# Optimization experiments

Measured on AMD Instinct MI355X. Metric: run time of the kernel, lower is better.

## Reference

```python
import jax, jax.numpy as jnp
import numpy as np

# NOTE: the original source omits the definitions of QSVT, quantum_lcu_block,
# QuantumSumBlock and KANLayer. We reconstruct the standard math these blocks
# implement in quantum-KAN papers/repos:
#   QSVT(x)            -> vector of Chebyshev polynomials T_1..T_D of the
#                         (squashed) input, the polynomial basis QSVT realizes.
#   quantum_lcu_block  -> linear combination of unitaries: weighted sum of the
#                         QSVT vector normalized by the LCU l1 weight norm.
#   QuantumSumBlock    -> learnable interference sum: mean_k sin(alpha_k * v).
#   KANLayer           -> Chebyshev-KAN layer: spline term (Chebyshev basis
#                         contracted with coeffs) + SiLU base branch + bias.
# Everything is fully vectorized over (B, F) instead of the original per-scalar
# Python loops.

B, F, DEG, C, KBASIS = 16384, 512, 8, 10, 8


def _cheb(x, K):
    """Chebyshev features T_1..T_K of x in (-1, 1): shape x.shape + (K,)."""
    t = jnp.arccos(jnp.clip(x, -1.0, 1.0))
    k = jnp.arange(1, K + 1, dtype=x.dtype)
    return jnp.cos(t[..., None] * k)


def setup_inputs() -> dict:
    key = jax.random.key(0)
    ks = jax.random.split(key, 6)
    return {
        "X": jax.random.normal(ks[0], (B, F), dtype=jnp.float32),
        # nn.Parameter(torch.rand(num_features, degree))
        "lcu_weights": jax.random.uniform(ks[1], (F, DEG), dtype=jnp.float32),
        # one QuantumSumBlock(degree) per feature -> (F, DEG) phases
        "sum_alpha": jax.random.normal(ks[2], (F, DEG), dtype=jnp.float32),
        # KANLayer params
        "kan_coeff": jax.random.normal(ks[3], (C, F, KBASIS), dtype=jnp.float32) * 0.1,
        "kan_base": jax.random.normal(ks[4], (C, F), dtype=jnp.float32) * 0.1,
        "kan_bias": jnp.zeros((C,), dtype=jnp.float32),
    }


def reference(X, lcu_weights, sum_alpha, kan_coeff, kan_base, kan_bias):
    # squash inputs into the open interval (-1, 1) for the Chebyshev/QSVT basis
    x = 0.99 * jnp.tanh(X)                                   # (B, F)
    # QSVT polynomial feature vector per scalar, batched: (B, F, DEG)
    qsvt = _cheb(x, lcu_weights.shape[1])
    # LCU block: weighted combination normalized by l1 norm of weights -> (B, F)
    lcu = jnp.einsum('bfd,fd->bf', qsvt, lcu_weights) / (
        jnp.sum(jnp.abs(lcu_weights), axis=-1) + 1e-8)
    # Quantum sum block: learnable sinusoidal interference sum -> (B, F)
    summed = jnp.mean(jnp.sin(lcu[..., None] * sum_alpha), axis=-1)
    # Chebyshev-KAN layer
    s = 0.99 * jnp.tanh(summed)
    phi = _cheb(s, kan_coeff.shape[2])                       # (B, F, KBASIS)
    logits = (jnp.einsum('bfk,cfk->bc', phi, kan_coeff)
              + jax.nn.silu(summed) @ kan_base.T
              + kan_bias)                                    # (B, C)
    return logits
```

## Files before the change

### kernel.cpp

```cpp
#include <hip/hip_runtime.h>

#define BATCH 16384
#define NF    512
#define DEG   8
#define NC    10
#define KB    8

#define SPLITF 8
#define FC     (NF / SPLITF)
#define RB     64
#define PITCH  65
#define NT     256
#define NWAVES 4
#define FPW    (FC / NWAVES)

__device__ __forceinline__ float fast_tanh(float x) {
    float e = __expf(2.0f * x);
    return 1.0f - 2.0f * __builtin_amdgcn_rcpf(e + 1.0f);
}
__device__ __forceinline__ float fast_sigmoid(float x) {
    return __builtin_amdgcn_rcpf(1.0f + __expf(-x));
}

__global__ __launch_bounds__(256) void init_out(const float* __restrict__ bias,
                                                float* __restrict__ out) {
    int i = blockIdx.x * 256 + threadIdx.x;
    if (i < BATCH * NC) out[i] = bias[i % NC];
}

__global__ __launch_bounds__(NT) void qkan_kernel(
    const float* __restrict__ X,
    const float* __restrict__ lcu_w,
    const float* __restrict__ alpha,
    const float* __restrict__ coeff,
    const float* __restrict__ base,
    float* __restrict__ out)
{
    __shared__ float s_mem[RB * PITCH];

    const int t      = threadIdx.x;
    const int rowblk = blockIdx.x >> 3;
    const int fsplit = blockIdx.x & (SPLITF - 1);
    const int row0   = rowblk * RB;
    const int fbase  = fsplit * FC;
    const int wave   = __builtin_amdgcn_readfirstlane(t >> 6);
    const int lane   = t & 63;

    {
        const int f2   = t & 31;
        const int rsub = t >> 5;
        const int fA   = fbase + f2 * 2;

        float w[2][DEG], a[2][DEG], rden[2];
#pragma unroll
        for (int i = 0; i < 2; ++i) {
            const float4 w0 = *(const float4*)(lcu_w + (fA + i) * DEG);
            const float4 w1 = *(const float4*)(lcu_w + (fA + i) * DEG + 4);
            const float4 a0 = *(const float4*)(alpha + (fA + i) * DEG);
            const float4 a1 = *(const float4*)(alpha + (fA + i) * DEG + 4);
            w[i][0]=w0.x; w[i][1]=w0.y; w[i][2]=w0.z; w[i][3]=w0.w;
            w[i][4]=w1.x; w[i][5]=w1.y; w[i][6]=w1.z; w[i][7]=w1.w;
            a[i][0]=a0.x; a[i][1]=a0.y; a[i][2]=a0.z; a[i][3]=a0.w;
            a[i][4]=a1.x; a[i][5]=a1.y; a[i][6]=a1.z; a[i][7]=a1.w;
            float den = 1e-8f;
#pragma unroll
            for (int d = 0; d < DEG; ++d) den += fabsf(w[i][d]);
            rden[i] = __builtin_amdgcn_rcpf(den);
        }

#pragma unroll
        for (int it = 0; it < RB / 8; ++it) {
            const int r = rsub + it * 8;
            const float2 xv = *(const float2*)(X + (row0 + r) * NF + fA);
            float xs[2] = {xv.x, xv.y};
#pragma unroll
            for (int i = 0; i < 2; ++i) {
                const float x  = 0.99f * fast_tanh(xs[i]);
                const float x2 = 2.0f * x;
                float tkm1 = 1.0f, tk = x, num = 0.0f;
#pragma unroll
                for (int d = 0; d < DEG; ++d) {
                    num = fmaf(w[i][d], tk, num);
                    float tn = fmaf(x2, tk, -tkm1);
                    tkm1 = tk; tk = tn;
                }
                const float lcu = num * rden[i];
                float ss = 0.0f;
#pragma unroll
                for (int d = 0; d < DEG; ++d)
                    ss += __sinf(lcu * a[i][d]);
                s_mem[r * PITCH + f2 * 2 + i] = 0.125f * ss;
            }
        }
    }
    __syncthreads();

    float acc[NC];
#pragma unroll
    for (int c = 0; c < NC; ++c) acc[c] = 0.0f;

#pragma unroll 2
    for (int j = 0; j < FPW; ++j) {
        const int foff = wave * FPW + j;
        const int f    = __builtin_amdgcn_readfirstlane(fbase + foff);
        const float sm = s_mem[lane * PITCH + foff];

        const float s   = 0.99f * fast_tanh(sm);
        const float sil = sm * fast_sigmoid(sm);

        float phi[KB];
        {
            float tkm1 = 1.0f, tk = s;
            const float s2 = 2.0f * s;
#pragma unroll
            for (int k = 0; k < KB; ++k) {
                phi[k] = tk;
                float tn = fmaf(s2, tk, -tkm1);
                tkm1 = tk; tk = tn;
            }
        }
#pragma unroll
        for (int c = 0; c < NC; ++c) {
            const float* cf = coeff + (c * NF + f) * KB;
            float v = acc[c];
#pragma unroll
            for (int k = 0; k < KB; ++k)
                v = fmaf(phi[k], cf[k], v);
            acc[c] = fmaf(sil, base[c * NF + f], v);
        }
    }
    __syncthreads();

#pragma unroll
    for (int c = 0; c < NC; ++c)
        s_mem[(wave * RB + lane) * NC + c] = acc[c];
    __syncthreads();

    for (int idx = t; idx < RB * NC; idx += NT) {
        const int r = idx / NC;
        const int c = idx - r * NC;
        float v = s_mem[idx];
#pragma unroll
        for (int w = 1; w < NWAVES; ++w)
            v += s_mem[(w * RB + r) * NC + c];
        unsafeAtomicAdd(out + (row0 + r) * NC + c, v);
    }
}

extern "C" void kernel_launch(void* const* d_in, const int* in_sizes, int n_in,
                              void* d_out, int out_size, void* d_ws, size_t ws_size,
                              hipStream_t stream) {
    const float* X      = (const float*)d_in[0];
    const float* lcu_w  = (const float*)d_in[1];
    const float* alpha  = (const float*)d_in[2];
    const float* coeff  = (const float*)d_in[3];
    const float* base   = (const float*)d_in[4];
    const float* bias   = (const float*)d_in[5];
    float* out = (float*)d_out;

    init_out<<<(BATCH * NC + 255) / 256, 256, 0, stream>>>(bias, out);
    qkan_kernel<<<(BATCH / RB) * SPLITF, NT, 0, stream>>>(X, lcu_w, alpha, coeff, base, out);
}
```

Before: 118.9 us.

## Compute KAN contraction with bf16 MFMA instead of scalar FMA loops

Replaces the per-lane scalar Chebyshev-KAN contraction with MFMA 16x16x32 bf16 matrix instructions. The Chebyshev features and SiLU values become the A operand and the coefficients and base weights become register-resident B fragments. The row block grows to 128 rows with a new shared-memory pitch, and the cross-wave shared reduction is removed so each wave atomically adds its own MFMA results. This trades float32 accuracy in the contraction for bf16 operands, which risks tolerance failures, and it pads the 10 output classes to 16 MFMA columns.

```diff
diff --git a/kernel.cpp b/kernel.cpp
--- a/kernel.cpp
+++ b/kernel.cpp
@@ -8,11 +8,15 @@
 
 #define SPLITF 8
 #define FC     (NF / SPLITF)
-#define RB     64
-#define PITCH  65
+#define RB     128
+#define PITCH  68
 #define NT     256
 #define NWAVES 4
-#define FPW    (FC / NWAVES)
+
+typedef __attribute__((ext_vector_type(8))) short bfrag;
+typedef __attribute__((ext_vector_type(4))) float f32x4;
+
+union frag_u { bfrag s; unsigned u[4]; };
 
 __device__ __forceinline__ float fast_tanh(float x) {
     float e = __expf(2.0f * x);
@@ -20,6 +24,26 @@
 }
 __device__ __forceinline__ float fast_sigmoid(float x) {
     return __builtin_amdgcn_rcpf(1.0f + __expf(-x));
+}
+__device__ __forceinline__ unsigned bfpack2(float lo, float hi) {
+    unsigned ul = __builtin_bit_cast(unsigned, lo) + 0x8000u;
+    unsigned uh = __builtin_bit_cast(unsigned, hi) + 0x8000u;
+    return __builtin_amdgcn_perm(uh, ul, 0x07060302);
+}
+__device__ __forceinline__ bfrag cheb_frag(float s) {
+    float T[KB];
+    float tkm1 = 1.0f, tk = s;
+    const float s2 = 2.0f * s;
+#pragma unroll
+    for (int k = 0; k < KB; ++k) {
+        T[k] = tk;
+        float tn = fmaf(s2, tk, -tkm1);
+        tkm1 = tk; tk = tn;
+    }
+    frag_u f;
+#pragma unroll
+    for (int i = 0; i < 4; ++i) f.u[i] = bfpack2(T[2 * i], T[2 * i + 1]);
+    return f.s;
 }
 
 __global__ __launch_bounds__(256) void init_out(const float* __restrict__ bias,
@@ -28,7 +52,7 @@
     if (i < BATCH * NC) out[i] = bias[i % NC];
 }
 
-__global__ __launch_bounds__(NT) void qkan_kernel(
+__global__ __launch_bounds__(NT, 4) void qkan_kernel(
     const float* __restrict__ X,
     const float* __restrict__ lcu_w,
     const float* __restrict__ alpha,
@@ -43,8 +67,6 @@
     const int fsplit = blockIdx.x & (SPLITF - 1);
     const int row0   = rowblk * RB;
     const int fbase  = fsplit * FC;
-    const int wave   = __builtin_amdgcn_readfirstlane(t >> 6);
-    const int lane   = t & 63;
 
     {
         const int f2   = t & 31;
@@ -73,6 +95,7 @@
             const int r = rsub + it * 8;
             const float2 xv = *(const float2*)(X + (row0 + r) * NF + fA);
             float xs[2] = {xv.x, xv.y};
+            float sums[2];
 #pragma unroll
             for (int i = 0; i < 2; ++i) {
                 const float x  = 0.99f * fast_tanh(xs[i]);
@@ -89,61 +112,92 @@
 #pragma unroll
                 for (int d = 0; d < DEG; ++d)
                     ss += __sinf(lcu * a[i][d]);
-                s_mem[r * PITCH + f2 * 2 + i] = 0.125f * ss;
+                sums[i] = 0.125f * ss;
             }
+            *(float2*)(&s_mem[r * PITCH + f2 * 2]) = make_float2(sums[0], sums[1]);
         }
     }
     __syncthreads();
 
-    float acc[NC];
-#pragma unroll
-    for (int c = 0; c < NC; ++c) acc[c] = 0.0f;
-
-#pragma unroll 2
-    for (int j = 0; j < FPW; ++j) {
-        const int foff = wave * FPW + j;
-        const int f    = __builtin_amdgcn_readfirstlane(fbase + foff);
-        const float sm = s_mem[lane * PITCH + foff];
-
-        const float s   = 0.99f * fast_tanh(sm);
-        const float sil = sm * fast_sigmoid(sm);
-
-        float phi[KB];
-        {
-            float tkm1 = 1.0f, tk = s;
-            const float s2 = 2.0f * s;
-#pragma unroll
-            for (int k = 0; k < KB; ++k) {
-                phi[k] = tk;
-                float tn = fmaf(s2, tk, -tkm1);
-                tkm1 = tk; tk = tn;
-            }
-        }
-#pragma unroll
-        for (int c = 0; c < NC; ++c) {
-            const float* cf = coeff + (c * NF + f) * KB;
-            float v = acc[c];
-#pragma unroll
-            for (int k = 0; k < KB; ++k)
-                v = fmaf(phi[k], cf[k], v);
-            acc[c] = fmaf(sil, base[c * NF + f], v);
-        }
-    }
-    __syncthreads();
-
-#pragma unroll
-    for (int c = 0; c < NC; ++c)
-        s_mem[(wave * RB + lane) * NC + c] = acc[c];
-    __syncthreads();
-
-    for (int idx = t; idx < RB * NC; idx += NT) {
-        const int r = idx / NC;
-        const int c = idx - r * NC;
-        float v = s_mem[idx];
-#pragma unroll
-        for (int w = 1; w < NWAVES; ++w)
-            v += s_mem[(w * RB + r) * NC + c];
-        unsafeAtomicAdd(out + (row0 + r) * NC + c, v);
+    const int lane = t & 63;
+    const int wave = __builtin_amdgcn_readfirstlane(t >> 6);
+    const int n    = lane & 15;
+    const int q    = lane >> 4;
+    const bool nv  = (n < NC);
+    const int  ncl = nv ? n : (NC - 1);
+
+    bfrag Bc[16];
+#pragma unroll
+    for (int kt = 0; kt < 16; ++kt) {
+        const float* p = coeff + (ncl * NF + fbase + kt * 4 + q) * KB;
+        float4 c0 = *(const float4*)p;
+        float4 c1 = *(const float4*)(p + 4);
+        if (!nv) { c0 = make_float4(0,0,0,0); c1 = make_float4(0,0,0,0); }
+        frag_u f;
+        f.u[0] = bfpack2(c0.x, c0.y); f.u[1] = bfpack2(c0.z, c0.w);
+        f.u[2] = bfpack2(c1.x, c1.y); f.u[3] = bfpack2(c1.z, c1.w);
+        Bc[kt] = f.s;
+    }
+    bfrag Bs[2];
+#pragma unroll
+    for (int kt2 = 0; kt2 < 2; ++kt2) {
+        const float* p = base + ncl * NF + fbase + kt2 * 32 + q * 8;
+        float4 b0 = *(const float4*)p;
+        float4 b1 = *(const float4*)(p + 4);
+        if (!nv) { b0 = make_float4(0,0,0,0); b1 = make_float4(0,0,0,0); }
+        frag_u f;
+        f.u[0] = bfpack2(b0.x, b0.y); f.u[1] = bfpack2(b0.z, b0.w);
+        f.u[2] = bfpack2(b1.x, b1.y); f.u[3] = bfpack2(b1.z, b1.w);
+        Bs[kt2] = f.s;
+    }
+
+    const int r_l0 = wave * 32 + n;
+    const int r_l1 = r_l0 + 16;
+
+    f32x4 acc0 = {0.f, 0.f, 0.f, 0.f};
+    f32x4 acc1 = {0.f, 0.f, 0.f, 0.f};
+
+#pragma unroll
+    for (int kt = 0; kt < 16; ++kt) {
+        const int fl = kt * 4 + q;
+        const float s0 = s_mem[r_l0 * PITCH + fl];
+        const float s1 = s_mem[r_l1 * PITCH + fl];
+        const bfrag a0 = cheb_frag(0.99f * fast_tanh(s0));
+        const bfrag a1 = cheb_frag(0.99f * fast_tanh(s1));
+        acc0 = __builtin_amdgcn_mfma_f32_16x16x32_bf16(a0, Bc[kt], acc0, 0, 0, 0);
+        acc1 = __builtin_amdgcn_mfma_f32_16x16x32_bf16(a1, Bc[kt], acc1, 0, 0, 0);
+    }
+
+#pragma unroll
+    for (int kt2 = 0; kt2 < 2; ++kt2) {
+        const int off = kt2 * 32 + q * 8;
+#pragma unroll
+        for (int tt = 0; tt < 2; ++tt) {
+            const int rl = (tt == 0) ? r_l0 : r_l1;
+            const float4 v0 = *(const float4*)(&s_mem[rl * PITCH + off]);
+            const float4 v1 = *(const float4*)(&s_mem[rl * PITCH + off + 4]);
+            float v[8] = {v0.x, v0.y, v0.z, v0.w, v1.x, v1.y, v1.z, v1.w};
+            float sl[8];
+#pragma unroll
+            for (int j = 0; j < 8; ++j)
+                sl[j] = v[j] * fast_sigmoid(v[j]);
+            frag_u f;
+            f.u[0] = bfpack2(sl[0], sl[1]); f.u[1] = bfpack2(sl[2], sl[3]);
+            f.u[2] = bfpack2(sl[4], sl[5]); f.u[3] = bfpack2(sl[6], sl[7]);
+            if (tt == 0)
+                acc0 = __builtin_amdgcn_mfma_f32_16x16x32_bf16(f.s, Bs[kt2], acc0, 0, 0, 0);
+            else
+                acc1 = __builtin_amdgcn_mfma_f32_16x16x32_bf16(f.s, Bs[kt2], acc1, 0, 0, 0);
+        }
+    }
+
+    if (nv) {
+#pragma unroll
+        for (int i = 0; i < 4; ++i) {
+            const int rg0 = row0 + wave * 32 + q * 4 + i;
+            unsafeAtomicAdd(out + rg0 * NC + n, acc0[i]);
+            unsafeAtomicAdd(out + (rg0 + 16) * NC + n, acc1[i]);
+        }
     }
 }
 
```

New measurement: 125.9 us. 5.9% more time.
